# Performance work log

Hardware: AMD Instinct MI355X
Metric: run time of the kernel (lower is better)

Reference implementation:

```python
import jax, jax.numpy as jnp
import numpy as np

EPS = 0.01  # eigenvalue cutoff in vstars_from_quadrics


def _cluster(predicted_points, samples, normals):
    # predicted_points: [B,M,3]; samples, normals: [B,N,3]
    B, N, _ = samples.shape
    M = predicted_points.shape[1]

    # --- knn_points with k=1: argmin_m ||s_n - p_m||^2 = argmin_m (|p_m|^2 - 2 s.p) ---
    dots = jnp.einsum('bnd,bmd->bnm', samples, predicted_points)      # [B,N,M]
    pp2 = jnp.sum(predicted_points * predicted_points, axis=-1)       # [B,M]
    closest_idx = jnp.argmin(pp2[:, None, :] - 2.0 * dots, axis=-1)   # [B,N] int

    # --- per-sample plane quadric (ps ps^T), ps = [n, -n.s] ---
    ds = -jnp.sum(normals * samples, axis=-1)                          # [B,N]
    ps = jnp.concatenate([normals, ds[..., None]], axis=-1)            # [B,N,4]
    quadrics = (ps[..., :, None] * ps[..., None, :]).reshape(B, N, 16)  # [B,N,16]

    # --- scatter_mean into M voronoi bins (zero default for empty bins) ---
    seg_sum = jax.vmap(lambda v, i: jax.ops.segment_sum(v, i, num_segments=M))
    q_sum = seg_sum(quadrics, closest_idx)                              # [B,M,16]
    n_sum = seg_sum(normals, closest_idx)                               # [B,M,3]
    cnt = seg_sum(jnp.ones((B, N, 1), quadrics.dtype), closest_idx)     # [B,M,1]
    denom = jnp.maximum(cnt, 1.0)
    target_quadrics = (q_sum / denom).reshape(B, M, 4, 4)
    mean_normals = n_sum / denom

    non_void = jnp.sum(mean_normals * mean_normals, axis=-1) > 0        # [B,M] bool

    # --- vstars_from_quadrics (computed densely, masked where bin is empty) ---
    A = target_quadrics[..., :3, :3]                                    # [B,M,3,3]
    bvec = -target_quadrics[..., 3, :3]                                 # [B,M,3]
    # void bins -> A == 0; substitute a well-conditioned matrix so SVD is safe,
    # result is masked to 0 anyway (rhs is 0 there as well).
    fake = jnp.diag(jnp.asarray([3.0, 2.0, 1.0], A.dtype))
    A_safe = jnp.where(non_void[..., None, None], A, fake)
    u, eigs, vh = jnp.linalg.svd(A_safe)                                # eigs desc
    ratio = eigs / jnp.maximum(eigs[..., 0:1], 1e-20)
    mask_s = ratio > EPS
    eigs2 = jnp.where(mask_s, 1.0 / jnp.where(mask_s, eigs, 1.0), 0.0)  # [B,M,3]
    rhs = bvec - jnp.einsum('bmij,bmj->bmi', A, predicted_points)       # b - A p
    t = jnp.einsum('bmji,bmj->bmi', u, rhs)                             # U^T rhs
    delta = jnp.einsum('bmji,bmj->bmi', vh, eigs2 * t)                  # Vh^T D U^T rhs
    vstars = predicted_points + delta
    vstars = jnp.where(non_void[..., None], vstars, 0.0)
    return A, mean_normals, vstars, non_void


def setup_inputs() -> dict:
    key = jax.random.key(0)
    k1, k2, k3 = jax.random.split(key, 3)
    B, M, N = 4, 1024, 65536
    predicted_points = jax.random.normal(k1, (B, M, 3), dtype=jnp.float32)
    samples = jax.random.normal(k2, (B, N, 3), dtype=jnp.float32)
    normals = jax.random.normal(k3, (B, N, 3), dtype=jnp.float32)
    normals = normals / jnp.linalg.norm(normals, axis=-1, keepdims=True)
    return {"predicted_points": predicted_points, "samples": samples, "normals": normals}


def reference(predicted_points, samples, normals):
    target_As, mean_normals, vstars, non_void = _cluster(predicted_points, samples, normals)
    return target_As, mean_normals, vstars, non_void
```

## Files before the change

### kernel.cpp

```cpp
#include <hip/hip_runtime.h>

#define BB 4
#define MM 1024
#define NN 65536
#define CL (BB * MM)

#define ROTJ(APP, AQQ, APQ, ARP, ARQ, V0P, V1P, V2P, V0Q, V1Q, V2Q)            \
    do {                                                                       \
        double apq_ = APQ;                                                     \
        if (fabs(apq_) > 1e-300) {                                             \
            double theta_ = (AQQ - APP) / (2.0 * apq_);                        \
            double t_ = 1.0 / (fabs(theta_) + sqrt(theta_ * theta_ + 1.0));    \
            if (theta_ < 0.0) t_ = -t_;                                        \
            double c_ = 1.0 / sqrt(t_ * t_ + 1.0), sn_ = t_ * c_;              \
            APP -= t_ * apq_; AQQ += t_ * apq_; APQ = 0.0;                     \
            double arp_ = ARP, arq_ = ARQ;                                     \
            ARP = c_ * arp_ - sn_ * arq_;                                      \
            ARQ = sn_ * arp_ + c_ * arq_;                                      \
            double x_;                                                         \
            x_ = V0P; V0P = c_ * x_ - sn_ * V0Q; V0Q = sn_ * x_ + c_ * V0Q;    \
            x_ = V1P; V1P = c_ * x_ - sn_ * V1Q; V1Q = sn_ * x_ + c_ * V1Q;    \
            x_ = V2P; V2P = c_ * x_ - sn_ * V2Q; V2Q = sn_ * x_ + c_ * V2Q;    \
        }                                                                      \
    } while (0)

#define CESWAP(EI, EJ, VA, VB, VC, WA, WB, WC)                                 \
    do {                                                                       \
        if (EI < EJ) {                                                         \
            double tt_;                                                        \
            tt_ = EI; EI = EJ; EJ = tt_;                                       \
            tt_ = VA; VA = WA; WA = tt_;                                       \
            tt_ = VB; VB = WB; WB = tt_;                                       \
            tt_ = VC; VC = WC; WC = tt_;                                       \
        }                                                                      \
    } while (0)

__global__ __launch_bounds__(256) void k_clear(int4* __restrict__ head4)
{
    head4[blockIdx.x * 256 + threadIdx.x] = make_int4(-1, -1, -1, -1);
}

__global__ __launch_bounds__(512) void k_assign(
    const float* __restrict__ pp, const float* __restrict__ smp,
    int* __restrict__ head, int* __restrict__ next)
{
    __shared__ float4 pts[MM];
    __shared__ float bestSh[8][256];
    __shared__ int   biSh[8][256];

    const int b   = blockIdx.x >> 8;
    const int blk = blockIdx.x & 255;
    const float* P = pp + b * MM * 3;
    for (int i = threadIdx.x; i < MM; i += 512) {
        float x = P[i * 3 + 0], y = P[i * 3 + 1], z = P[i * 3 + 2];
        pts[i] = make_float4(x, y, z, x * x + y * y + z * z);
    }
    __syncthreads();

    const int l  = threadIdx.x & 63;
    const int g  = threadIdx.x >> 6;
    const int nb = blk * 256;
    const float* S = smp + (size_t)b * NN * 3;

    float ax[4], ay[4], az[4], best[4];
    int bi[4];
#pragma unroll
    for (int j = 0; j < 4; ++j) {
        int n = nb + j * 64 + l;
        ax[j] = -2.0f * S[n * 3 + 0];
        ay[j] = -2.0f * S[n * 3 + 1];
        az[j] = -2.0f * S[n * 3 + 2];
        best[j] = 3.4e38f;
        bi[j] = 0;
    }
    const int m0 = g * 128;
#pragma unroll 4
    for (int mi = 0; mi < 128; ++mi) {
        float4 p = pts[m0 + mi];
#pragma unroll
        for (int j = 0; j < 4; ++j) {
            float sc = fmaf(ax[j], p.x, fmaf(ay[j], p.y, fmaf(az[j], p.z, p.w)));
            if (sc < best[j]) { best[j] = sc; bi[j] = m0 + mi; }
        }
    }
#pragma unroll
    for (int j = 0; j < 4; ++j) {
        bestSh[g][j * 64 + l] = best[j];
        biSh[g][j * 64 + l]   = bi[j];
    }
    __syncthreads();

    if (threadIdx.x < 256) {
        const int t = threadIdx.x;
        float bb = bestSh[0][t];
        int   ii = biSh[0][t];
#pragma unroll
        for (int gg = 1; gg < 8; ++gg) {
            float bo = bestSh[gg][t];
            int   io = biSh[gg][t];
            if (bo < bb) { bb = bo; ii = io; }
        }
        const int n = nb + t;
        const int gc = b * MM + ii;
        next[(size_t)b * NN + n] = atomicExch(&head[gc * 64 + (t & 63)], n);
    }
}

__global__ __launch_bounds__(256) void k_cluster(
    const float* __restrict__ pp, const float* __restrict__ smp,
    const float* __restrict__ nrm, const int* __restrict__ head,
    const int* __restrict__ next, float* __restrict__ out)
{
    __shared__ double sums[4][14];

    const int wid  = threadIdx.x >> 6;
    const int lane = threadIdx.x & 63;
    const int wave = blockIdx.x * 4 + wid;
    const int bc = wave >> 10;
    const int* NX = next + (size_t)bc * NN;
    const float* Sc = smp + (size_t)bc * NN * 3;
    const float* Nr = nrm + (size_t)bc * NN * 3;

    double q00 = 0, q01 = 0, q02 = 0, q11 = 0, q12 = 0, q22 = 0;
    double nd0 = 0, nd1 = 0, nd2 = 0, s0 = 0, s1 = 0, s2 = 0;
    int count = 0;

    int cur = head[wave * 64 + lane];
    while (cur >= 0) {
        double sxv = Sc[cur * 3 + 0], syv = Sc[cur * 3 + 1], szv = Sc[cur * 3 + 2];
        double nx = Nr[cur * 3 + 0], ny = Nr[cur * 3 + 1], nz = Nr[cur * 3 + 2];
        double d = -(nx * sxv + ny * syv + nz * szv);
        q00 += nx * nx; q01 += nx * ny; q02 += nx * nz;
        q11 += ny * ny; q12 += ny * nz; q22 += nz * nz;
        nd0 += nx * d; nd1 += ny * d; nd2 += nz * d;
        s0 += nx; s1 += ny; s2 += nz;
        ++count;
        cur = NX[cur];
    }
#pragma unroll
    for (int o = 32; o > 0; o >>= 1) {
        q00 += __shfl_xor(q00, o); q01 += __shfl_xor(q01, o); q02 += __shfl_xor(q02, o);
        q11 += __shfl_xor(q11, o); q12 += __shfl_xor(q12, o); q22 += __shfl_xor(q22, o);
        nd0 += __shfl_xor(nd0, o); nd1 += __shfl_xor(nd1, o); nd2 += __shfl_xor(nd2, o);
        s0  += __shfl_xor(s0, o);  s1  += __shfl_xor(s1, o);  s2  += __shfl_xor(s2, o);
        count += __shfl_xor(count, o);
    }
    if (lane == 0) {
        sums[wid][0] = q00; sums[wid][1] = q01; sums[wid][2] = q02;
        sums[wid][3] = q11; sums[wid][4] = q12; sums[wid][5] = q22;
        sums[wid][6] = nd0; sums[wid][7] = nd1; sums[wid][8] = nd2;
        sums[wid][9] = s0;  sums[wid][10] = s1; sums[wid][11] = s2;
        sums[wid][12] = (double)count;
    }
    __syncthreads();

    if (threadIdx.x < 4) {
        const int c = blockIdx.x * 4 + threadIdx.x;
        const double* t = sums[threadIdx.x];
        const int cnt = (int)t[12];

        double denom = cnt > 1 ? (double)cnt : 1.0;
        double A00 = t[0] / denom, A01 = t[1] / denom, A02 = t[2] / denom;
        double A11 = t[3] / denom, A12 = t[4] / denom, A22 = t[5] / denom;
        double bv0 = -t[6] / denom, bv1 = -t[7] / denom, bv2 = -t[8] / denom;
        double mn0 = t[9] / denom, mn1 = t[10] / denom, mn2 = t[11] / denom;
        bool nonvoid = (mn0 * mn0 + mn1 * mn1 + mn2 * mn2) > 0.0;

        double vs0 = 0, vs1 = 0, vs2 = 0;
        if (nonvoid) {
            double a00 = A00, a01 = A01, a02 = A02, a11 = A11, a12 = A12, a22 = A22;
            double v00 = 1, v01 = 0, v02 = 0;
            double v10 = 0, v11 = 1, v12 = 0;
            double v20 = 0, v21 = 0, v22 = 1;
#pragma unroll
            for (int sweep = 0; sweep < 8; ++sweep) {
                ROTJ(a00, a11, a01, a02, a12, v00, v10, v20, v01, v11, v21);
                ROTJ(a00, a22, a02, a01, a12, v00, v10, v20, v02, v12, v22);
                ROTJ(a11, a22, a12, a01, a02, v01, v11, v21, v02, v12, v22);
            }
            double e0 = a00, e1 = a11, e2 = a22;
            CESWAP(e0, e1, v00, v10, v20, v01, v11, v21);
            CESWAP(e0, e2, v00, v10, v20, v02, v12, v22);
            CESWAP(e1, e2, v01, v11, v21, v02, v12, v22);

            double emax = e0 > 1e-20 ? e0 : 1e-20;
            const float* Pp = pp + (size_t)c * 3;
            double px = Pp[0], py = Pp[1], pz = Pp[2];
            double r0 = bv0 - (A00 * px + A01 * py + A02 * pz);
            double r1 = bv1 - (A01 * px + A11 * py + A12 * pz);
            double r2 = bv2 - (A02 * px + A12 * py + A22 * pz);
            double thr = 0.01 * emax;
            if (e0 > thr) { double w = (v00 * r0 + v10 * r1 + v20 * r2) / e0; vs0 += w * v00; vs1 += w * v10; vs2 += w * v20; }
            if (e1 > thr) { double w = (v01 * r0 + v11 * r1 + v21 * r2) / e1; vs0 += w * v01; vs1 += w * v11; vs2 += w * v21; }
            if (e2 > thr) { double w = (v02 * r0 + v12 * r1 + v22 * r2) / e2; vs0 += w * v02; vs1 += w * v12; vs2 += w * v22; }
            vs0 += px; vs1 += py; vs2 += pz;
        }

        float* Ao = out + (size_t)c * 9;
        Ao[0] = (float)A00; Ao[1] = (float)A01; Ao[2] = (float)A02;
        Ao[3] = (float)A01; Ao[4] = (float)A11; Ao[5] = (float)A12;
        Ao[6] = (float)A02; Ao[7] = (float)A12; Ao[8] = (float)A22;
        float* Mo = out + 36864 + (size_t)c * 3;
        Mo[0] = (float)mn0; Mo[1] = (float)mn1; Mo[2] = (float)mn2;
        float* Vo = out + 49152 + (size_t)c * 3;
        Vo[0] = (float)vs0; Vo[1] = (float)vs1; Vo[2] = (float)vs2;
        out[61440 + c] = nonvoid ? 1.0f : 0.0f;
    }
}

extern "C" void kernel_launch(void* const* d_in, const int* in_sizes, int n_in,
                              void* d_out, int out_size, void* d_ws, size_t ws_size,
                              hipStream_t stream)
{
    const float* pp  = (const float*)d_in[0];
    const float* smp = (const float*)d_in[1];
    const float* nrm = (const float*)d_in[2];
    float* out = (float*)d_out;

    int* head = (int*)d_ws;
    int* next = head + CL * 64;

    k_clear<<<256, 256, 0, stream>>>((int4*)head);
    k_assign<<<1024, 512, 0, stream>>>(pp, smp, head, next);
    k_cluster<<<CL / 4, 256, 0, stream>>>(pp, smp, nrm, head, next, out);
}
```

Baseline: 72.48 us.

## Replace per-cluster linked lists with fixed-capacity bucketed plane payload arrays

The assign kernel now computes each sample's plane vector (normal plus offset d) and appends it to a per-cluster bucket via atomicAdd, using a non-temporal store. This replaces the atomicExch linked list. The cluster kernel then reads each bucket with coalesced, lane-strided loads instead of chasing dependent next pointers through the samples and normals arrays. This removes the serial pointer-chasing latency and the scattered gathers. In exchange it uses a large fixed workspace, and any cluster receiving more than 1024 samples would silently drop the excess from its sums.

```diff
diff --git a/kernel.cpp b/kernel.cpp
--- a/kernel.cpp
+++ b/kernel.cpp
@@ -4,6 +4,9 @@
 #define MM 1024
 #define NN 65536
 #define CL (BB * MM)
+#define CAP 1024
+
+typedef float fvec4 __attribute__((ext_vector_type(4)));
 
 #define ROTJ(APP, AQQ, APQ, ARP, ARQ, V0P, V1P, V2P, V0Q, V1Q, V2Q)            \
     do {                                                                       \
@@ -35,14 +38,15 @@
         }                                                                      \
     } while (0)
 
-__global__ __launch_bounds__(256) void k_clear(int4* __restrict__ head4)
-{
-    head4[blockIdx.x * 256 + threadIdx.x] = make_int4(-1, -1, -1, -1);
+__global__ __launch_bounds__(256) void k_clear_cnt(int4* __restrict__ cnt4)
+{
+    cnt4[blockIdx.x * 256 + threadIdx.x] = make_int4(0, 0, 0, 0);
 }
 
 __global__ __launch_bounds__(512) void k_assign(
     const float* __restrict__ pp, const float* __restrict__ smp,
-    int* __restrict__ head, int* __restrict__ next)
+    const float* __restrict__ nrm, int* __restrict__ cnt,
+    fvec4* __restrict__ payload)
 {
     __shared__ float4 pts[MM];
     __shared__ float bestSh[8][256];
@@ -102,40 +106,42 @@
         }
         const int n = nb + t;
         const int gc = b * MM + ii;
-        next[(size_t)b * NN + n] = atomicExch(&head[gc * 64 + (t & 63)], n);
+
+        const float* Nr = nrm + (size_t)b * NN * 3;
+        float sx = S[n * 3 + 0], sy = S[n * 3 + 1], sz = S[n * 3 + 2];
+        float nx = Nr[n * 3 + 0], ny = Nr[n * 3 + 1], nz = Nr[n * 3 + 2];
+        float d = -(nx * sx + ny * sy + nz * sz);
+        fvec4 pl;
+        pl[0] = nx; pl[1] = ny; pl[2] = nz; pl[3] = d;
+
+        int pos = atomicAdd(&cnt[gc], 1);
+        if (pos < CAP)
+            __builtin_nontemporal_store(pl, &payload[((size_t)gc << 10) + pos]);
     }
 }
 
 __global__ __launch_bounds__(256) void k_cluster(
-    const float* __restrict__ pp, const float* __restrict__ smp,
-    const float* __restrict__ nrm, const int* __restrict__ head,
-    const int* __restrict__ next, float* __restrict__ out)
+    const float* __restrict__ pp, const fvec4* __restrict__ payload,
+    const int* __restrict__ cnt, float* __restrict__ out)
 {
     __shared__ double sums[4][14];
 
     const int wid  = threadIdx.x >> 6;
     const int lane = threadIdx.x & 63;
     const int wave = blockIdx.x * 4 + wid;
-    const int bc = wave >> 10;
-    const int* NX = next + (size_t)bc * NN;
-    const float* Sc = smp + (size_t)bc * NN * 3;
-    const float* Nr = nrm + (size_t)bc * NN * 3;
+    const int count = cnt[wave];
+    const int stored = count < CAP ? count : CAP;
+    const fvec4* PL = payload + ((size_t)wave << 10);
 
     double q00 = 0, q01 = 0, q02 = 0, q11 = 0, q12 = 0, q22 = 0;
     double nd0 = 0, nd1 = 0, nd2 = 0, s0 = 0, s1 = 0, s2 = 0;
-    int count = 0;
-
-    int cur = head[wave * 64 + lane];
-    while (cur >= 0) {
-        double sxv = Sc[cur * 3 + 0], syv = Sc[cur * 3 + 1], szv = Sc[cur * 3 + 2];
-        double nx = Nr[cur * 3 + 0], ny = Nr[cur * 3 + 1], nz = Nr[cur * 3 + 2];
-        double d = -(nx * sxv + ny * syv + nz * szv);
+    for (int i = lane; i < stored; i += 64) {
+        fvec4 pl = PL[i];
+        double nx = pl[0], ny = pl[1], nz = pl[2], d = pl[3];
         q00 += nx * nx; q01 += nx * ny; q02 += nx * nz;
         q11 += ny * ny; q12 += ny * nz; q22 += nz * nz;
         nd0 += nx * d; nd1 += ny * d; nd2 += nz * d;
         s0 += nx; s1 += ny; s2 += nz;
-        ++count;
-        cur = NX[cur];
     }
 #pragma unroll
     for (int o = 32; o > 0; o >>= 1) {
@@ -143,7 +149,6 @@
         q11 += __shfl_xor(q11, o); q12 += __shfl_xor(q12, o); q22 += __shfl_xor(q22, o);
         nd0 += __shfl_xor(nd0, o); nd1 += __shfl_xor(nd1, o); nd2 += __shfl_xor(nd2, o);
         s0  += __shfl_xor(s0, o);  s1  += __shfl_xor(s1, o);  s2  += __shfl_xor(s2, o);
-        count += __shfl_xor(count, o);
     }
     if (lane == 0) {
         sums[wid][0] = q00; sums[wid][1] = q01; sums[wid][2] = q02;
@@ -157,9 +162,9 @@
     if (threadIdx.x < 4) {
         const int c = blockIdx.x * 4 + threadIdx.x;
         const double* t = sums[threadIdx.x];
-        const int cnt = (int)t[12];
-
-        double denom = cnt > 1 ? (double)cnt : 1.0;
+        const int cn = (int)t[12];
+
+        double denom = cn > 1 ? (double)cn : 1.0;
         double A00 = t[0] / denom, A01 = t[1] / denom, A02 = t[2] / denom;
         double A11 = t[3] / denom, A12 = t[4] / denom, A22 = t[5] / denom;
         double bv0 = -t[6] / denom, bv1 = -t[7] / denom, bv2 = -t[8] / denom;
@@ -217,10 +222,10 @@
     const float* nrm = (const float*)d_in[2];
     float* out = (float*)d_out;
 
-    int* head = (int*)d_ws;
-    int* next = head + CL * 64;
-
-    k_clear<<<256, 256, 0, stream>>>((int4*)head);
-    k_assign<<<1024, 512, 0, stream>>>(pp, smp, head, next);
-    k_cluster<<<CL / 4, 256, 0, stream>>>(pp, smp, nrm, head, next, out);
-}
+    int*   cnt     = (int*)d_ws;
+    fvec4* payload = (fvec4*)((char*)d_ws + 65536);
+
+    k_clear_cnt<<<4, 256, 0, stream>>>((int4*)cnt);
+    k_assign<<<1024, 512, 0, stream>>>(pp, smp, nrm, cnt, payload);
+    k_cluster<<<CL / 4, 256, 0, stream>>>(pp, payload, cnt, out);
+}
```

After: 87.33 us. 1.2x slower.
